# Performance work log

Hardware: AMD Instinct MI355X
Metric: run time of the kernel (lower is better)

The kernel has to match this reference:

```python
import jax, jax.numpy as jnp
import numpy as np
from jax import lax

EPS = 1e-6
MATCH_THRESHOLD = 0.3
N_DISCRETE_STEPS = 5
DT = 0.01
TWO_PI = 2.0 * np.pi


def setup_inputs() -> dict:
    key = jax.random.key(0)
    ks = jax.random.split(key, 6)
    N, M, D, H, n_osc = 8192, 8192, 4, 64, 28
    detections_t = jax.random.normal(ks[0], (N, D), dtype=jnp.float32)
    detections_t1 = jax.random.normal(ks[1], (M, D), dtype=jnp.float32)
    phase_W1 = jax.random.normal(ks[2], (D, H), dtype=jnp.float32) * (1.0 / np.sqrt(D))
    phase_b1 = jax.random.normal(ks[3], (H,), dtype=jnp.float32) * 0.05
    phase_W2 = jax.random.normal(ks[4], (H, n_osc), dtype=jnp.float32) * (1.0 / np.sqrt(H))
    phase_b2 = jax.random.normal(ks[5], (n_osc,), dtype=jnp.float32) * 0.05
    # fixed oscillator frequencies buffer: [2]*4 + [6]*8 + [40]*16
    frequencies = jnp.concatenate([
        jnp.full((4,), 2.0, jnp.float32),
        jnp.full((8,), 6.0, jnp.float32),
        jnp.full((16,), 40.0, jnp.float32),
    ])
    return {
        'detections_t': detections_t,
        'detections_t1': detections_t1,
        'phase_W1': phase_W1,
        'phase_b1': phase_b1,
        'phase_W2': phase_W2,
        'phase_b2': phase_b2,
        'frequencies': frequencies,
    }


def _encode_phase(x, W1, b1, W2, b2):
    h = jax.nn.relu(x @ W1 + b1)
    raw = h @ W2 + b2
    return raw % TWO_PI  # [N, n_osc]


def _similarity(phase_a, phase_b):
    # real(sum_k e^{i a_k} e^{-i b_k}) = cos(a)@cos(b).T + sin(a)@sin(b).T
    ca, sa = jnp.cos(phase_a), jnp.sin(phase_a)
    cb, sb = jnp.cos(phase_b), jnp.sin(phase_b)
    na = jnp.sqrt(jnp.sum(ca * ca + sa * sa, axis=-1, keepdims=True)) + EPS  # [N,1]
    nb = jnp.sqrt(jnp.sum(cb * cb + sb * sb, axis=-1, keepdims=True)) + EPS  # [M,1]
    sim = (ca @ cb.T + sa @ sb.T) / (na * nb.T)  # [N, M]
    return sim


def reference(detections_t, detections_t1, phase_W1, phase_b1, phase_W2, phase_b2, frequencies):
    phase_t = _encode_phase(detections_t, phase_W1, phase_b1, phase_W2, phase_b2)
    phase_t1 = _encode_phase(detections_t1, phase_W1, phase_b1, phase_W2, phase_b2)

    # uncoupled phase advance (n_discrete_steps fixed small loop)
    phase = phase_t
    for _ in range(N_DISCRETE_STEPS):
        phase = (phase + TWO_PI * frequencies * DT) % TWO_PI

    sim = _similarity(phase, phase_t1)  # [N, M]

    N = detections_t.shape[0]
    M = detections_t1.shape[0]
    max_sims = jnp.max(sim, axis=1)
    max_idxs = jnp.argmax(sim, axis=1)
    order = jnp.argsort(-max_sims)  # descending

    def body(i, carry):
        matches, used = carry
        idx = order[i]
        j = max_idxs[idx]
        ok = jnp.logical_and(jnp.logical_not(used[j]), max_sims[idx] > MATCH_THRESHOLD)
        matches = matches.at[idx].set(jnp.where(ok, j, -1))
        used = used.at[j].set(jnp.logical_or(used[j], ok))
        return (matches, used)

    matches0 = jnp.full((N,), -1, dtype=jnp.int32)
    used0 = jnp.zeros((M,), dtype=bool)
    matches, _ = lax.fori_loop(0, N, body, (matches0, used0))
    return (matches, sim)
```

## Files before the change

### kernel.cpp

```cpp
#include <hip/hip_runtime.h>
#include <math.h>

#define NR 8192
#define N_OSC 28
#define TWO_PI_F 6.28318530717958647692f
#define PLANE 524288

typedef __attribute__((ext_vector_type(8))) short s16x8;
typedef __attribute__((ext_vector_type(16))) float f32x16;
typedef __attribute__((ext_vector_type(4))) float f32x4;

#define AS3(p) ((__attribute__((address_space(3))) void*)(p))
#define AS1C(p) ((const __attribute__((address_space(1))) void*)(p))

__device__ __forceinline__ float modpos(float x) {
    float r = fmodf(x, TWO_PI_F);
    if (r < 0.0f) r += TWO_PI_F;
    return r;
}
__device__ __forceinline__ unsigned fmono(float f) {
    unsigned u = __float_as_uint(f);
    return (u & 0x80000000u) ? ~u : (u | 0x80000000u);
}
__device__ __forceinline__ unsigned short f2bf(float f) {
    unsigned u = __float_as_uint(f);
    return (unsigned short)((u + 0x7FFFu + ((u >> 16) & 1u)) >> 16);
}
__device__ __forceinline__ float bf2f(unsigned short h) {
    return __uint_as_float(((unsigned)h) << 16);
}

__global__ __launch_bounds__(256) void encode_kernel(
    const float* __restrict__ detA, const float* __restrict__ detB,
    const float* __restrict__ W1, const float* __restrict__ b1,
    const float* __restrict__ W2, const float* __restrict__ b2,
    const float* __restrict__ freq,
    unsigned short* __restrict__ tabA, unsigned short* __restrict__ tabB,
    float* __restrict__ normA, float* __restrict__ normB)
{
    __shared__ float sW1[4 * 64];
    __shared__ float sb1[64];
    __shared__ float sW2[64 * N_OSC];
    __shared__ float sb2[N_OSC];
    __shared__ float sDelta[N_OSC];

    int t = threadIdx.x;
    for (int i = t; i < 4 * 64; i += 256) sW1[i] = W1[i];
    for (int i = t; i < 64; i += 256) sb1[i] = b1[i];
    for (int i = t; i < 64 * N_OSC; i += 256) sW2[i] = W2[i];
    for (int i = t; i < N_OSC; i += 256) {
        sb2[i] = b2[i];
        sDelta[i] = (TWO_PI_F * freq[i]) * 0.01f;
    }
    __syncthreads();

    int gid = blockIdx.x * 256 + t;
    bool isA = gid < NR;
    int row = isA ? gid : gid - NR;
    const float* det = isA ? detA : detB;
    unsigned short* tab = isA ? tabA : tabB;
    float* nrm = isA ? normA : normB;

    float4 xv = *(const float4*)(det + (size_t)row * 4);
    float x0 = xv.x, x1 = xv.y, x2 = xv.z, x3 = xv.w;

    float h[64];
#pragma unroll
    for (int j = 0; j < 64; ++j) {
        float a = x0 * sW1[0 * 64 + j];
        a += x1 * sW1[1 * 64 + j];
        a += x2 * sW1[2 * 64 + j];
        a += x3 * sW1[3 * 64 + j];
        a += sb1[j];
        h[j] = fmaxf(a, 0.0f);
    }

    float raw[N_OSC];
#pragma unroll
    for (int o = 0; o < N_OSC; ++o) raw[o] = 0.0f;
#pragma unroll
    for (int j = 0; j < 64; ++j) {
        float hj = h[j];
#pragma unroll
        for (int o = 0; o < N_OSC; ++o) raw[o] += hj * sW2[j * N_OSC + o];
    }

    int rs = row & 7;
    size_t rbase = (size_t)row * 64;
    float csum = 0.0f;
#pragma unroll
    for (int o = 0; o < N_OSC; ++o) {
        float p = raw[o] + sb2[o];
        p = modpos(p);
        if (isA) {
            float d = sDelta[o];
#pragma unroll
            for (int s = 0; s < 5; ++s) { p = modpos(p + d); }
        }
        float sn, cs;
        sincosf(p, &sn, &cs);
        csum += cs * cs + sn * sn;
        {
            int k = o;
            unsigned short h0 = f2bf(cs); float r1 = cs - bf2f(h0);
            unsigned short h1 = f2bf(r1); float r2 = r1 - bf2f(h1);
            unsigned short h2 = f2bf(r2);
            size_t e = rbase + ((((k >> 3) ^ rs) << 3) | (k & 7));
            tab[e] = h0; tab[PLANE + e] = h1; tab[2 * PLANE + e] = h2;
        }
        {
            int k = 28 + o;
            unsigned short h0 = f2bf(sn); float r1 = sn - bf2f(h0);
            unsigned short h1 = f2bf(r1); float r2 = r1 - bf2f(h1);
            unsigned short h2 = f2bf(r2);
            size_t e = rbase + ((((k >> 3) ^ rs) << 3) | (k & 7));
            tab[e] = h0; tab[PLANE + e] = h1; tab[2 * PLANE + e] = h2;
        }
    }
#pragma unroll
    for (int k = 56; k < 64; ++k) {
        size_t e = rbase + ((((k >> 3) ^ rs) << 3) | (k & 7));
        tab[e] = 0; tab[PLANE + e] = 0; tab[2 * PLANE + e] = 0;
    }
    nrm[row] = 1.0f / (sqrtf(csum) + 1e-6f);
}

__device__ __forceinline__ void stage_plane(const unsigned short* __restrict__ tab,
                                            int dim0, unsigned short* dst,
                                            int w, int l)
{
#pragma unroll
    for (int i = 0; i < 4; ++i) {
        int u = w * 4 + i;
        const unsigned short* g = tab + (size_t)(dim0 + 8 * u + (l >> 3)) * 64 + (l & 7) * 8;
        __builtin_amdgcn_global_load_lds(AS1C(g), AS3(dst + u * 512), 16, 0, 0);
    }
}

__global__ __launch_bounds__(256) void sim_kernel(
    const unsigned short* __restrict__ tabA, const unsigned short* __restrict__ tabB,
    const float* __restrict__ normA, const float* __restrict__ normB,
    float* __restrict__ simOut, unsigned long long* __restrict__ rowMax)
{
    __shared__ __align__(16) unsigned char smem[81920];
    unsigned short* Bsh0 = (unsigned short*)(smem);
    unsigned short* Bsh1 = (unsigned short*)(smem + 16384);
    unsigned short* Bsh2 = (unsigned short*)(smem + 32768);
    unsigned short* Ash0 = (unsigned short*)(smem + 49152);
    unsigned short* Ash1 = (unsigned short*)(smem + 65536);

    int bid = blockIdx.x;
    int swz = (bid & 7) * 512 + (bid >> 3);
    int bx = swz & 63, by = swz >> 6;
    int r0 = by * 128, c0 = bx * 128;

    int t = threadIdx.x, w = t >> 6, l = t & 63;
    int wr = w >> 1, wc = w & 1;
    int lrow = l & 31;
    int kh2 = (l >> 5) * 16;
    int sw = (lrow & 7) << 4;

    stage_plane(tabB, c0, Bsh0, w, l);
    stage_plane(tabB + PLANE, c0, Bsh1, w, l);
    stage_plane(tabB + 2 * PLANE, c0, Bsh2, w, l);
    stage_plane(tabA, r0, Ash0, w, l);
    __syncthreads();
    stage_plane(tabA + PLANE, r0, Ash1, w, l);

    f32x16 acc00, acc01, acc10, acc11;
#pragma unroll
    for (int r = 0; r < 16; ++r) { acc00[r] = 0.f; acc01[r] = 0.f; acc10[r] = 0.f; acc11[r] = 0.f; }

    int baA0 = (wr * 64 + lrow) * 128, baA1 = baA0 + 32 * 128;
    int baB0 = (wc * 64 + lrow) * 128, baB1 = baB0 + 32 * 128;

#define FR(arr, ba, ks) (*(const s16x8*)((const char*)(arr) + (ba) + (((ks) * 32 + kh2) ^ sw)))

    s16x8 bh0[4], bh1[4];

#pragma unroll
    for (int ks = 0; ks < 4; ++ks) {
        s16x8 a0 = FR(Ash0, baA0, ks), a1 = FR(Ash0, baA1, ks);
        bh0[ks] = FR(Bsh0, baB0, ks); bh1[ks] = FR(Bsh0, baB1, ks);
        acc00 = __builtin_amdgcn_mfma_f32_32x32x16_bf16(a0, bh0[ks], acc00, 0, 0, 0);
        acc01 = __builtin_amdgcn_mfma_f32_32x32x16_bf16(a0, bh1[ks], acc01, 0, 0, 0);
        acc10 = __builtin_amdgcn_mfma_f32_32x32x16_bf16(a1, bh0[ks], acc10, 0, 0, 0);
        acc11 = __builtin_amdgcn_mfma_f32_32x32x16_bf16(a1, bh1[ks], acc11, 0, 0, 0);
        s16x8 b0 = FR(Bsh1, baB0, ks), b1 = FR(Bsh1, baB1, ks);
        acc00 = __builtin_amdgcn_mfma_f32_32x32x16_bf16(a0, b0, acc00, 0, 0, 0);
        acc01 = __builtin_amdgcn_mfma_f32_32x32x16_bf16(a0, b1, acc01, 0, 0, 0);
        acc10 = __builtin_amdgcn_mfma_f32_32x32x16_bf16(a1, b0, acc10, 0, 0, 0);
        acc11 = __builtin_amdgcn_mfma_f32_32x32x16_bf16(a1, b1, acc11, 0, 0, 0);
        b0 = FR(Bsh2, baB0, ks); b1 = FR(Bsh2, baB1, ks);
        acc00 = __builtin_amdgcn_mfma_f32_32x32x16_bf16(a0, b0, acc00, 0, 0, 0);
        acc01 = __builtin_amdgcn_mfma_f32_32x32x16_bf16(a0, b1, acc01, 0, 0, 0);
        acc10 = __builtin_amdgcn_mfma_f32_32x32x16_bf16(a1, b0, acc10, 0, 0, 0);
        acc11 = __builtin_amdgcn_mfma_f32_32x32x16_bf16(a1, b1, acc11, 0, 0, 0);
    }
    __syncthreads();
    stage_plane(tabA + 2 * PLANE, r0, Ash0, w, l);

#pragma unroll
    for (int ks = 0; ks < 4; ++ks) {
        s16x8 a0 = FR(Ash1, baA0, ks), a1 = FR(Ash1, baA1, ks);
        acc00 = __builtin_amdgcn_mfma_f32_32x32x16_bf16(a0, bh0[ks], acc00, 0, 0, 0);
        acc01 = __builtin_amdgcn_mfma_f32_32x32x16_bf16(a0, bh1[ks], acc01, 0, 0, 0);
        acc10 = __builtin_amdgcn_mfma_f32_32x32x16_bf16(a1, bh0[ks], acc10, 0, 0, 0);
        acc11 = __builtin_amdgcn_mfma_f32_32x32x16_bf16(a1, bh1[ks], acc11, 0, 0, 0);
        s16x8 b0 = FR(Bsh1, baB0, ks), b1 = FR(Bsh1, baB1, ks);
        acc00 = __builtin_amdgcn_mfma_f32_32x32x16_bf16(a0, b0, acc00, 0, 0, 0);
        acc01 = __builtin_amdgcn_mfma_f32_32x32x16_bf16(a0, b1, acc01, 0, 0, 0);
        acc10 = __builtin_amdgcn_mfma_f32_32x32x16_bf16(a1, b0, acc10, 0, 0, 0);
        acc11 = __builtin_amdgcn_mfma_f32_32x32x16_bf16(a1, b1, acc11, 0, 0, 0);
    }
    __syncthreads();

#pragma unroll
    for (int ks = 0; ks < 4; ++ks) {
        s16x8 a0 = FR(Ash0, baA0, ks), a1 = FR(Ash0, baA1, ks);
        acc00 = __builtin_amdgcn_mfma_f32_32x32x16_bf16(a0, bh0[ks], acc00, 0, 0, 0);
        acc01 = __builtin_amdgcn_mfma_f32_32x32x16_bf16(a0, bh1[ks], acc01, 0, 0, 0);
        acc10 = __builtin_amdgcn_mfma_f32_32x32x16_bf16(a1, bh0[ks], acc10, 0, 0, 0);
        acc11 = __builtin_amdgcn_mfma_f32_32x32x16_bf16(a1, bh1[ks], acc11, 0, 0, 0);
    }
#undef FR

    float icn0 = normB[c0 + wc * 64 + lrow];
    float icn1 = normB[c0 + wc * 64 + 32 + lrow];

    __syncthreads();
    float* scr = (float*)(smem + w * 17408);

#pragma unroll
    for (int r = 0; r < 16; ++r) {
        int rd0 = (r & 3) + 8 * (r >> 2) + 4 * (l >> 5);
        float irn0 = normA[r0 + wr * 64 + rd0];
        scr[rd0 * 68 + lrow]      = acc00[r] * (irn0 * icn0);
        scr[rd0 * 68 + 32 + lrow] = acc01[r] * (irn0 * icn1);
        int rd1 = rd0 + 32;
        float irn1 = normA[r0 + wr * 64 + rd1];
        scr[rd1 * 68 + lrow]      = acc10[r] * (irn1 * icn0);
        scr[rd1 * 68 + 32 + lrow] = acc11[r] * (irn1 * icn1);
    }

#pragma unroll
    for (int s = 0; s < 16; ++s) {
        int lr = 4 * s + (l >> 4);
        f32x4 v = *(const f32x4*)&scr[lr * 68 + (l & 15) * 4];
        int grow = r0 + wr * 64 + lr;
        __builtin_nontemporal_store(v,
            (f32x4*)&simOut[(size_t)grow * NR + c0 + wc * 64 + (l & 15) * 4]);
    }

    {
        const float* rp = &scr[l * 68];
        float mv = -2.0f; int mc = 0;
#pragma unroll
        for (int c4 = 0; c4 < 16; ++c4) {
            f32x4 v = *(const f32x4*)&rp[c4 * 4];
#pragma unroll
            for (int e = 0; e < 4; ++e) {
                bool g = v[e] > mv;
                mv = g ? v[e] : mv;
                mc = g ? c4 * 4 + e : mc;
            }
        }
        int grow = r0 + wr * 64 + l;
        unsigned gcol = (unsigned)(c0 + wc * 64 + mc);
        unsigned long long key = ((unsigned long long)fmono(mv) << 32)
                               | (unsigned long long)(0xFFFFFFFFu - gcol);
        atomicMax(&rowMax[grow], key);
    }
}

__global__ __launch_bounds__(256) void rowwin_kernel(
    const unsigned long long* __restrict__ rowMax,
    unsigned long long* __restrict__ colWin,
    float* __restrict__ outMatches)
{
    int r = blockIdx.x * 256 + threadIdx.x;
    if (r >= NR) return;
    outMatches[r] = -1.0f;
    unsigned long long key = rowMax[r];
    unsigned m = (unsigned)(key >> 32);
    unsigned bits = (m & 0x80000000u) ? (m ^ 0x80000000u) : ~m;
    float ms = __uint_as_float(bits);
    unsigned col = 0xFFFFFFFFu - (unsigned)key;
    if (ms > 0.3f) {
        unsigned long long ck = ((unsigned long long)m << 32)
                              | (unsigned long long)(0xFFFFFFFFu - (unsigned)r);
        atomicMax(&colWin[col], ck);
    }
}

__global__ __launch_bounds__(256) void colfin_kernel(
    const unsigned long long* __restrict__ colWin,
    float* __restrict__ outMatches)
{
    int j = blockIdx.x * 256 + threadIdx.x;
    if (j >= NR) return;
    unsigned long long w = colWin[j];
    if (w != 0ull) {
        unsigned r = 0xFFFFFFFFu - (unsigned)w;
        outMatches[r] = (float)j;
    }
}

extern "C" void kernel_launch(void* const* d_in, const int* in_sizes, int n_in,
                              void* d_out, int out_size, void* d_ws, size_t ws_size,
                              hipStream_t stream) {
    const float* detA = (const float*)d_in[0];
    const float* detB = (const float*)d_in[1];
    const float* W1   = (const float*)d_in[2];
    const float* b1   = (const float*)d_in[3];
    const float* W2   = (const float*)d_in[4];
    const float* b2   = (const float*)d_in[5];
    const float* freq = (const float*)d_in[6];
    float* out = (float*)d_out;

    char* ws = (char*)d_ws;
    unsigned short* tabA = (unsigned short*)(ws);
    unsigned short* tabB = (unsigned short*)(ws + 3145728);
    float* normA = (float*)(ws + 6291456);
    float* normB = (float*)(ws + 6324224);
    unsigned long long* rowMax = (unsigned long long*)(ws + 6356992);
    unsigned long long* colWin = (unsigned long long*)(ws + 6422528);

    (void)hipMemsetAsync(rowMax, 0, NR * 8, stream);
    (void)hipMemsetAsync(colWin, 0, NR * 8, stream);

    encode_kernel<<<64, 256, 0, stream>>>(detA, detB, W1, b1, W2, b2, freq,
                                          tabA, tabB, normA, normB);
    sim_kernel<<<4096, 256, 0, stream>>>(tabA, tabB, normA, normB, out + NR, rowMax);
    rowwin_kernel<<<NR / 256, 256, 0, stream>>>(rowMax, colWin, out);
    colfin_kernel<<<NR / 256, 256, 0, stream>>>(colWin, out);
}
```

Baseline: 132.9 us.

## Pre-swizzle tables into MFMA fragment layout and load operands directly from global

The encode kernel now packs the three bf16 split planes into registers and writes them in a layout that matches the MFMA fragment order: 32-row groups, with 16-byte vectors per lane. The sim kernel drops the LDS staging, the barriers and the global_load_lds copies, and loads each A/B fragment straight from global memory (served from L2/L1). This removes the shared-memory round trip and the synchronisation, at the cost of redundant global loads across waves and no explicit prefetch. The six MFMA products per k-step are the same as before, only reordered. Encode also gets launch_bounds(256,1).

```diff
diff --git a/kernel.cpp b/kernel.cpp
--- a/kernel.cpp
+++ b/kernel.cpp
@@ -9,9 +9,7 @@
 typedef __attribute__((ext_vector_type(8))) short s16x8;
 typedef __attribute__((ext_vector_type(16))) float f32x16;
 typedef __attribute__((ext_vector_type(4))) float f32x4;
-
-#define AS3(p) ((__attribute__((address_space(3))) void*)(p))
-#define AS1C(p) ((const __attribute__((address_space(1))) void*)(p))
+typedef __attribute__((ext_vector_type(4))) unsigned int u32x4;
 
 __device__ __forceinline__ float modpos(float x) {
     float r = fmodf(x, TWO_PI_F);
@@ -30,7 +28,8 @@
     return __uint_as_float(((unsigned)h) << 16);
 }
 
-__global__ __launch_bounds__(256) void encode_kernel(
+
+__global__ __launch_bounds__(256, 1) void encode_kernel(
     const float* __restrict__ detA, const float* __restrict__ detB,
     const float* __restrict__ W1, const float* __restrict__ b1,
     const float* __restrict__ W2, const float* __restrict__ b2,
@@ -85,8 +84,10 @@
         for (int o = 0; o < N_OSC; ++o) raw[o] += hj * sW2[j * N_OSC + o];
     }
 
-    int rs = row & 7;
-    size_t rbase = (size_t)row * 64;
+    unsigned h2[32], m2[32], l2[32];
+#pragma unroll
+    for (int i = 0; i < 32; ++i) { h2[i] = 0u; m2[i] = 0u; l2[i] = 0u; }
+
     float csum = 0.0f;
 #pragma unroll
     for (int o = 0; o < N_OSC; ++o) {
@@ -101,53 +102,49 @@
         sincosf(p, &sn, &cs);
         csum += cs * cs + sn * sn;
         {
-            int k = o;
-            unsigned short h0 = f2bf(cs); float r1 = cs - bf2f(h0);
-            unsigned short h1 = f2bf(r1); float r2 = r1 - bf2f(h1);
-            unsigned short h2 = f2bf(r2);
-            size_t e = rbase + ((((k >> 3) ^ rs) << 3) | (k & 7));
-            tab[e] = h0; tab[PLANE + e] = h1; tab[2 * PLANE + e] = h2;
+            unsigned short v0 = f2bf(cs); float r1 = cs - bf2f(v0);
+            unsigned short v1 = f2bf(r1); float r2 = r1 - bf2f(v1);
+            unsigned short v2 = f2bf(r2);
+            const int k = o, i = k >> 1, sh = (k & 1) * 16;
+            h2[i] |= ((unsigned)v0) << sh;
+            m2[i] |= ((unsigned)v1) << sh;
+            l2[i] |= ((unsigned)v2) << sh;
         }
         {
-            int k = 28 + o;
-            unsigned short h0 = f2bf(sn); float r1 = sn - bf2f(h0);
-            unsigned short h1 = f2bf(r1); float r2 = r1 - bf2f(h1);
-            unsigned short h2 = f2bf(r2);
-            size_t e = rbase + ((((k >> 3) ^ rs) << 3) | (k & 7));
-            tab[e] = h0; tab[PLANE + e] = h1; tab[2 * PLANE + e] = h2;
-        }
-    }
-#pragma unroll
-    for (int k = 56; k < 64; ++k) {
-        size_t e = rbase + ((((k >> 3) ^ rs) << 3) | (k & 7));
-        tab[e] = 0; tab[PLANE + e] = 0; tab[2 * PLANE + e] = 0;
+            unsigned short v0 = f2bf(sn); float r1 = sn - bf2f(v0);
+            unsigned short v1 = f2bf(r1); float r2 = r1 - bf2f(v1);
+            unsigned short v2 = f2bf(r2);
+            const int k = 28 + o, i = k >> 1, sh = (k & 1) * 16;
+            h2[i] |= ((unsigned)v0) << sh;
+            m2[i] |= ((unsigned)v1) << sh;
+            l2[i] |= ((unsigned)v2) << sh;
+        }
+    }
+
+    size_t gbase = (size_t)(row >> 5) * 2048 + (size_t)(row & 31) * 8;
+#pragma unroll
+    for (int c = 0; c < 8; ++c) {
+        size_t off = gbase + (size_t)(c >> 1) * 512 + (size_t)(c & 1) * 256;
+        u32x4 vh, vm, vl;
+#pragma unroll
+        for (int e = 0; e < 4; ++e) {
+            vh[e] = h2[c * 4 + e]; vm[e] = m2[c * 4 + e]; vl[e] = l2[c * 4 + e];
+        }
+        *(u32x4*)(tab + off) = vh;
+        *(u32x4*)(tab + PLANE + off) = vm;
+        *(u32x4*)(tab + 2 * PLANE + off) = vl;
     }
     nrm[row] = 1.0f / (sqrtf(csum) + 1e-6f);
 }
 
-__device__ __forceinline__ void stage_plane(const unsigned short* __restrict__ tab,
-                                            int dim0, unsigned short* dst,
-                                            int w, int l)
-{
-#pragma unroll
-    for (int i = 0; i < 4; ++i) {
-        int u = w * 4 + i;
-        const unsigned short* g = tab + (size_t)(dim0 + 8 * u + (l >> 3)) * 64 + (l & 7) * 8;
-        __builtin_amdgcn_global_load_lds(AS1C(g), AS3(dst + u * 512), 16, 0, 0);
-    }
-}
+#define MFMA(a, b, c) __builtin_amdgcn_mfma_f32_32x32x16_bf16((a), (b), (c), 0, 0, 0)
 
 __global__ __launch_bounds__(256) void sim_kernel(
     const unsigned short* __restrict__ tabA, const unsigned short* __restrict__ tabB,
     const float* __restrict__ normA, const float* __restrict__ normB,
     float* __restrict__ simOut, unsigned long long* __restrict__ rowMax)
 {
-    __shared__ __align__(16) unsigned char smem[81920];
-    unsigned short* Bsh0 = (unsigned short*)(smem);
-    unsigned short* Bsh1 = (unsigned short*)(smem + 16384);
-    unsigned short* Bsh2 = (unsigned short*)(smem + 32768);
-    unsigned short* Ash0 = (unsigned short*)(smem + 49152);
-    unsigned short* Ash1 = (unsigned short*)(smem + 65536);
+    __shared__ __align__(16) float scrAll[4][64 * 68];
 
     int bid = blockIdx.x;
     int swz = (bid & 7) * 512 + (bid >> 3);
@@ -157,79 +154,45 @@
     int t = threadIdx.x, w = t >> 6, l = t & 63;
     int wr = w >> 1, wc = w & 1;
     int lrow = l & 31;
-    int kh2 = (l >> 5) * 16;
-    int sw = (lrow & 7) << 4;
-
-    stage_plane(tabB, c0, Bsh0, w, l);
-    stage_plane(tabB + PLANE, c0, Bsh1, w, l);
-    stage_plane(tabB + 2 * PLANE, c0, Bsh2, w, l);
-    stage_plane(tabA, r0, Ash0, w, l);
-    __syncthreads();
-    stage_plane(tabA + PLANE, r0, Ash1, w, l);
+    int gA = (r0 + wr * 64) >> 5;
+    int gB = (c0 + wc * 64) >> 5;
+    size_t l8 = (size_t)l * 8;
+
+#define LD(tab, pl, g, ks) \
+    (*(const s16x8*)((tab) + (size_t)(pl) * PLANE + (size_t)(g) * 2048 + (size_t)(ks) * 512 + l8))
 
     f32x16 acc00, acc01, acc10, acc11;
 #pragma unroll
     for (int r = 0; r < 16; ++r) { acc00[r] = 0.f; acc01[r] = 0.f; acc10[r] = 0.f; acc11[r] = 0.f; }
 
-    int baA0 = (wr * 64 + lrow) * 128, baA1 = baA0 + 32 * 128;
-    int baB0 = (wc * 64 + lrow) * 128, baB1 = baB0 + 32 * 128;
-
-#define FR(arr, ba, ks) (*(const s16x8*)((const char*)(arr) + (ba) + (((ks) * 32 + kh2) ^ sw)))
-
-    s16x8 bh0[4], bh1[4];
-
 #pragma unroll
     for (int ks = 0; ks < 4; ++ks) {
-        s16x8 a0 = FR(Ash0, baA0, ks), a1 = FR(Ash0, baA1, ks);
-        bh0[ks] = FR(Bsh0, baB0, ks); bh1[ks] = FR(Bsh0, baB1, ks);
-        acc00 = __builtin_amdgcn_mfma_f32_32x32x16_bf16(a0, bh0[ks], acc00, 0, 0, 0);
-        acc01 = __builtin_amdgcn_mfma_f32_32x32x16_bf16(a0, bh1[ks], acc01, 0, 0, 0);
-        acc10 = __builtin_amdgcn_mfma_f32_32x32x16_bf16(a1, bh0[ks], acc10, 0, 0, 0);
-        acc11 = __builtin_amdgcn_mfma_f32_32x32x16_bf16(a1, bh1[ks], acc11, 0, 0, 0);
-        s16x8 b0 = FR(Bsh1, baB0, ks), b1 = FR(Bsh1, baB1, ks);
-        acc00 = __builtin_amdgcn_mfma_f32_32x32x16_bf16(a0, b0, acc00, 0, 0, 0);
-        acc01 = __builtin_amdgcn_mfma_f32_32x32x16_bf16(a0, b1, acc01, 0, 0, 0);
-        acc10 = __builtin_amdgcn_mfma_f32_32x32x16_bf16(a1, b0, acc10, 0, 0, 0);
-        acc11 = __builtin_amdgcn_mfma_f32_32x32x16_bf16(a1, b1, acc11, 0, 0, 0);
-        b0 = FR(Bsh2, baB0, ks); b1 = FR(Bsh2, baB1, ks);
-        acc00 = __builtin_amdgcn_mfma_f32_32x32x16_bf16(a0, b0, acc00, 0, 0, 0);
-        acc01 = __builtin_amdgcn_mfma_f32_32x32x16_bf16(a0, b1, acc01, 0, 0, 0);
-        acc10 = __builtin_amdgcn_mfma_f32_32x32x16_bf16(a1, b0, acc10, 0, 0, 0);
-        acc11 = __builtin_amdgcn_mfma_f32_32x32x16_bf16(a1, b1, acc11, 0, 0, 0);
-    }
-    __syncthreads();
-    stage_plane(tabA + 2 * PLANE, r0, Ash0, w, l);
-
-#pragma unroll
-    for (int ks = 0; ks < 4; ++ks) {
-        s16x8 a0 = FR(Ash1, baA0, ks), a1 = FR(Ash1, baA1, ks);
-        acc00 = __builtin_amdgcn_mfma_f32_32x32x16_bf16(a0, bh0[ks], acc00, 0, 0, 0);
-        acc01 = __builtin_amdgcn_mfma_f32_32x32x16_bf16(a0, bh1[ks], acc01, 0, 0, 0);
-        acc10 = __builtin_amdgcn_mfma_f32_32x32x16_bf16(a1, bh0[ks], acc10, 0, 0, 0);
-        acc11 = __builtin_amdgcn_mfma_f32_32x32x16_bf16(a1, bh1[ks], acc11, 0, 0, 0);
-        s16x8 b0 = FR(Bsh1, baB0, ks), b1 = FR(Bsh1, baB1, ks);
-        acc00 = __builtin_amdgcn_mfma_f32_32x32x16_bf16(a0, b0, acc00, 0, 0, 0);
-        acc01 = __builtin_amdgcn_mfma_f32_32x32x16_bf16(a0, b1, acc01, 0, 0, 0);
-        acc10 = __builtin_amdgcn_mfma_f32_32x32x16_bf16(a1, b0, acc10, 0, 0, 0);
-        acc11 = __builtin_amdgcn_mfma_f32_32x32x16_bf16(a1, b1, acc11, 0, 0, 0);
-    }
-    __syncthreads();
-
-#pragma unroll
-    for (int ks = 0; ks < 4; ++ks) {
-        s16x8 a0 = FR(Ash0, baA0, ks), a1 = FR(Ash0, baA1, ks);
-        acc00 = __builtin_amdgcn_mfma_f32_32x32x16_bf16(a0, bh0[ks], acc00, 0, 0, 0);
-        acc01 = __builtin_amdgcn_mfma_f32_32x32x16_bf16(a0, bh1[ks], acc01, 0, 0, 0);
-        acc10 = __builtin_amdgcn_mfma_f32_32x32x16_bf16(a1, bh0[ks], acc10, 0, 0, 0);
-        acc11 = __builtin_amdgcn_mfma_f32_32x32x16_bf16(a1, bh1[ks], acc11, 0, 0, 0);
-    }
-#undef FR
+        s16x8 ah0 = LD(tabA, 0, gA, ks),     ah1 = LD(tabA, 0, gA + 1, ks);
+        s16x8 bh0 = LD(tabB, 0, gB, ks),     bh1 = LD(tabB, 0, gB + 1, ks);
+        s16x8 am0 = LD(tabA, 1, gA, ks),     am1 = LD(tabA, 1, gA + 1, ks);
+        s16x8 bm0 = LD(tabB, 1, gB, ks),     bm1 = LD(tabB, 1, gB + 1, ks);
+        s16x8 al0 = LD(tabA, 2, gA, ks),     al1 = LD(tabA, 2, gA + 1, ks);
+        s16x8 bl0 = LD(tabB, 2, gB, ks),     bl1 = LD(tabB, 2, gB + 1, ks);
+
+        acc00 = MFMA(ah0, bh0, acc00); acc01 = MFMA(ah0, bh1, acc01);
+        acc10 = MFMA(ah1, bh0, acc10); acc11 = MFMA(ah1, bh1, acc11);
+        acc00 = MFMA(ah0, bm0, acc00); acc01 = MFMA(ah0, bm1, acc01);
+        acc10 = MFMA(ah1, bm0, acc10); acc11 = MFMA(ah1, bm1, acc11);
+        acc00 = MFMA(am0, bh0, acc00); acc01 = MFMA(am0, bh1, acc01);
+        acc10 = MFMA(am1, bh0, acc10); acc11 = MFMA(am1, bh1, acc11);
+        acc00 = MFMA(am0, bm0, acc00); acc01 = MFMA(am0, bm1, acc01);
+        acc10 = MFMA(am1, bm0, acc10); acc11 = MFMA(am1, bm1, acc11);
+        acc00 = MFMA(ah0, bl0, acc00); acc01 = MFMA(ah0, bl1, acc01);
+        acc10 = MFMA(ah1, bl0, acc10); acc11 = MFMA(ah1, bl1, acc11);
+        acc00 = MFMA(al0, bh0, acc00); acc01 = MFMA(al0, bh1, acc01);
+        acc10 = MFMA(al1, bh0, acc10); acc11 = MFMA(al1, bh1, acc11);
+    }
+#undef LD
 
     float icn0 = normB[c0 + wc * 64 + lrow];
     float icn1 = normB[c0 + wc * 64 + 32 + lrow];
 
-    __syncthreads();
-    float* scr = (float*)(smem + w * 17408);
+    float* scr = scrAll[w];
 
 #pragma unroll
     for (int r = 0; r < 16; ++r) {
```

Result: slower. 150.3 us (+13.1%).
